# Kernel optimization log

Hardware: AMD Instinct MI355X
Metric: run time of the kernel (lower is better)

## Reference

```python
import jax, jax.numpy as jnp
import numpy as np

B, L, D, H, SD = 8, 1024, 768, 12, 5
DK = D // H
PAD = 256  # last PAD keys are padding


def _lin(key, fan_in, fan_out):
    kw, kb = jax.random.split(key)
    s = 1.0 / np.sqrt(fan_in)
    w = jax.random.uniform(kw, (fan_in, fan_out), jnp.float32, -s, s)
    b = jax.random.uniform(kb, (fan_out,), jnp.float32, -s, s)
    return w, b


def setup_inputs() -> dict:
    key = jax.random.key(0)
    ks = jax.random.split(key, 10)
    w_q, b_q = _lin(ks[0], D, D)
    w_k, b_k = _lin(ks[1], D, D)
    w_v, b_v = _lin(ks[2], D, D)
    w_fc, b_fc = _lin(ks[3], D, D)
    w_loc, b_loc = _lin(ks[4], SD, H)
    return {
        'q': jax.random.normal(ks[5], (B, L, D), jnp.float32),
        'k': jax.random.normal(ks[6], (B, L, D), jnp.float32),
        'v': jax.random.normal(ks[7], (B, L, D), jnp.float32),
        'pairwise_locs': jax.random.normal(ks[8], (B, L, L, SD), jnp.float32),
        'key_padding_mask': jnp.broadcast_to(jnp.arange(L) >= (L - PAD), (B, L)),
        'w_q': w_q, 'b_q': b_q, 'w_k': w_k, 'b_k': b_k,
        'w_v': w_v, 'b_v': b_v, 'w_fc': w_fc, 'b_fc': b_fc,
        'w_loc': w_loc, 'b_loc': b_loc,
        'ln_g': jnp.ones((D,), jnp.float32), 'ln_b': jnp.zeros((D,), jnp.float32),
    }


def _split_heads(x):  # [b, t, D] -> [h, b, t, dk]
    b, t, _ = x.shape
    return x.reshape(b, t, H, DK).transpose(2, 0, 1, 3)


def reference(q, k, v, pairwise_locs, key_padding_mask,
              w_q, b_q, w_k, b_k, w_v, b_v, w_fc, b_fc,
              w_loc, b_loc, ln_g, ln_b):
    residual = q
    qh = _split_heads(q @ w_q + b_q)   # h b l k
    kh = _split_heads(k @ w_k + b_k)   # h b t k
    vh = _split_heads(v @ w_v + b_v)   # h b t v
    scale = 1.0 / jnp.sqrt(jnp.asarray(DK, qh.dtype))
    attn = jnp.einsum('hblk,hbtk->hblt', qh, kh) * scale
    # pairwise_loc_fc: [b,l,t,sd] @ [sd,h] + b -> rearrange to h b l t; 'mul' fusion uses relu
    loc_attn = jax.nn.relu(jnp.einsum('bltd,dh->hblt', pairwise_locs, w_loc)
                           + b_loc[:, None, None, None])
    m = key_padding_mask[None, :, None, :]  # h b l t broadcast
    attn = jnp.where(m, -jnp.inf, attn)
    loc_attn = jnp.where(m, 0.0, loc_attn)
    fused_attn = jax.nn.softmax(jnp.log(jnp.clip(loc_attn, 1e-6)) + attn, axis=3)
    out = jnp.einsum('hblt,hbtv->hblv', fused_attn, vh)
    out = out.transpose(1, 2, 0, 3).reshape(q.shape[0], q.shape[1], D)
    out = out @ w_fc + b_fc  # dropout is identity in eval
    x = out + residual
    mu = jnp.mean(x, -1, keepdims=True)
    var = jnp.var(x, -1, keepdims=True)
    out = (x - mu) / jnp.sqrt(var + 1e-5) * ln_g + ln_b
    return (out, fused_attn)
```

## Files before the change

kernel.cpp:

```cpp
#include <hip/hip_runtime.h>
#include <hip/hip_bf16.h>

constexpr int B_  = 8;
constexpr int L_  = 1024;
constexpr int D_  = 768;
constexpr int H_  = 12;
constexpr int DK_ = 64;
constexpr int SD_ = 5;
constexpr int VALID_ = 768;

constexpr float SSCALE_ = 0.18033688011112042f;

typedef __attribute__((ext_vector_type(8))) __bf16 bf16x8;
typedef __attribute__((ext_vector_type(4))) float floatx4;

__device__ __forceinline__ unsigned short f2bf(float f) {
    unsigned int u = __float_as_uint(f);
    unsigned int r = (u + 0x7FFFu + ((u >> 16) & 1u)) >> 16;
    return (unsigned short)r;
}

__device__ __forceinline__ void g2l16(const void* g, void* l) {
    __builtin_amdgcn_global_load_lds(
        (const __attribute__((address_space(1))) void*)g,
        (__attribute__((address_space(3))) void*)l, 16, 0, 0);
}

__global__ __launch_bounds__(256) void cvt3_kernel(
    const float* __restrict__ x0, const float* __restrict__ x1,
    const float* __restrict__ x2,
    unsigned short* __restrict__ o0, unsigned short* __restrict__ o1,
    unsigned short* __restrict__ o2)
{
    const int w = blockIdx.y;
    const float* x = (w == 0) ? x0 : (w == 1) ? x1 : x2;
    unsigned short* o = (w == 0) ? o0 : (w == 1) ? o1 : o2;
    size_t i = ((size_t)blockIdx.x * 256 + threadIdx.x) * 8;
    float4 a = *(const float4*)(x + i);
    float4 b = *(const float4*)(x + i + 4);
    ushort4 q1; q1.x = f2bf(a.x); q1.y = f2bf(a.y); q1.z = f2bf(a.z); q1.w = f2bf(a.w);
    ushort4 q2; q2.x = f2bf(b.x); q2.y = f2bf(b.y); q2.z = f2bf(b.z); q2.w = f2bf(b.w);
    *(ushort4*)(o + i) = q1;
    *(ushort4*)(o + i + 4) = q2;
}

__global__ __launch_bounds__(256) void wt4_kernel(
    const float* __restrict__ W0, const float* __restrict__ W1,
    const float* __restrict__ W2, const float* __restrict__ W3,
    unsigned short* __restrict__ T0, unsigned short* __restrict__ T1,
    unsigned short* __restrict__ T2, unsigned short* __restrict__ T3)
{
    const int w = blockIdx.z;
    const float* W = (w == 0) ? W0 : (w == 1) ? W1 : (w == 2) ? W2 : W3;
    unsigned short* Wt = (w == 0) ? T0 : (w == 1) ? T1 : (w == 2) ? T2 : T3;
    __shared__ float tl[64][65];
    const int k0 = blockIdx.x * 64, n0 = blockIdx.y * 64;
    const int tid = threadIdx.x;
    #pragma unroll
    for (int i = 0; i < 4; i++) {
        int c = tid + i * 256;
        int r = c >> 4, c4 = (c & 15) * 4;
        float4 v = *(const float4*)(W + (size_t)(k0 + r) * D_ + n0 + c4);
        tl[r][c4] = v.x; tl[r][c4 + 1] = v.y; tl[r][c4 + 2] = v.z; tl[r][c4 + 3] = v.w;
    }
    __syncthreads();
    #pragma unroll
    for (int i = 0; i < 4; i++) {
        int c = tid + i * 256;
        int n_ = c >> 4, k4 = (c & 15) * 4;
        ushort4 o;
        o.x = f2bf(tl[k4 + 0][n_]); o.y = f2bf(tl[k4 + 1][n_]);
        o.z = f2bf(tl[k4 + 2][n_]); o.w = f2bf(tl[k4 + 3][n_]);
        *(ushort4*)(Wt + (size_t)(n0 + n_) * D_ + k0 + k4) = o;
    }
}

__global__ __launch_bounds__(256) void vt_kernel(
    const unsigned short* __restrict__ Vh, unsigned short* __restrict__ Vt)
{
    __shared__ unsigned short tl[64][65];
    const int t0 = blockIdx.x * 64, hb = blockIdx.y;
    const int tid = threadIdx.x;
    const unsigned short* src = Vh + (size_t)hb * L_ * DK_ + (size_t)t0 * DK_;
    #pragma unroll
    for (int i = 0; i < 4; i++) {
        int c = tid + i * 256;
        int r = c >> 4, c4 = (c & 15) * 4;
        ushort4 v = *(const ushort4*)(src + r * DK_ + c4);
        tl[r][c4] = v.x; tl[r][c4 + 1] = v.y; tl[r][c4 + 2] = v.z; tl[r][c4 + 3] = v.w;
    }
    __syncthreads();
    unsigned short* dst = Vt + (size_t)hb * DK_ * VALID_ + t0;
    #pragma unroll
    for (int i = 0; i < 4; i++) {
        int c = tid + i * 256;
        int dk = c >> 4, t4 = (c & 15) * 4;
        ushort4 o;
        o.x = tl[t4 + 0][dk]; o.y = tl[t4 + 1][dk];
        o.z = tl[t4 + 2][dk]; o.w = tl[t4 + 3][dk];
        *(ushort4*)(dst + (size_t)dk * VALID_ + t4) = o;
    }
}

__global__ __launch_bounds__(256) void gemm_proj3(
    const unsigned short* __restrict__ A0, const unsigned short* __restrict__ A1,
    const unsigned short* __restrict__ A2,
    const unsigned short* __restrict__ B0, const unsigned short* __restrict__ B1,
    const unsigned short* __restrict__ B2,
    const float* __restrict__ bias0, const float* __restrict__ bias1,
    const float* __restrict__ bias2,
    unsigned short* __restrict__ O0, unsigned short* __restrict__ O1,
    unsigned short* __restrict__ O2)
{
    const int which = blockIdx.z;
    const unsigned short* Abf = (which == 0) ? A0 : (which == 1) ? A1 : A2;
    const unsigned short* Bt  = (which == 0) ? B0 : (which == 1) ? B1 : B2;
    const float* bias         = (which == 0) ? bias0 : (which == 1) ? bias1 : bias2;
    unsigned short* out       = (which == 0) ? O0 : (which == 1) ? O1 : O2;

    __shared__ __align__(16) __bf16 As[128 * 32];
    __shared__ __align__(16) __bf16 Bs[128 * 32];
    const int tid = threadIdx.x;
    const int f = blockIdx.x + 6 * blockIdx.y;
    const int xcd = f & 7, j5 = f >> 3;
    const int n0 = (j5 % 6) * 128;
    const int m0 = (xcd * 8 + j5 / 6) * 128;
    const int lane = tid & 63, wv = tid >> 6;
    const int quad = lane >> 4, ln15 = lane & 15;
    const int wm = (wv >> 1) * 64, wn = (wv & 1) * 64;
    const __bf16* Ap = (const __bf16*)Abf + (size_t)m0 * D_;
    const __bf16* Bp = (const __bf16*)Bt + (size_t)n0 * D_;
    floatx4 acc[4][4];
    #pragma unroll
    for (int i = 0; i < 4; i++)
        #pragma unroll
        for (int j = 0; j < 4; j++) acc[i][j] = (floatx4)0.f;

    for (int k0 = 0; k0 < D_; k0 += 32) {
        #pragma unroll
        for (int j = 0; j < 2; j++) {
            int c = tid + j * 256;
            g2l16(Ap + (size_t)(c >> 2) * D_ + k0 + (c & 3) * 8, As + c * 8);
            g2l16(Bp + (size_t)(c >> 2) * D_ + k0 + (c & 3) * 8, Bs + c * 8);
        }
        __syncthreads();
        bf16x8 af[4], bfr[4];
        #pragma unroll
        for (int i = 0; i < 4; i++)
            af[i] = *(const bf16x8*)(As + (wm + i * 16 + ln15) * 32 + quad * 8);
        #pragma unroll
        for (int i = 0; i < 4; i++)
            bfr[i] = *(const bf16x8*)(Bs + (wn + i * 16 + ln15) * 32 + quad * 8);
        #pragma unroll
        for (int i = 0; i < 4; i++)
            #pragma unroll
            for (int j = 0; j < 4; j++)
                acc[i][j] = __builtin_amdgcn_mfma_f32_16x16x32_bf16(af[i], bfr[j], acc[i][j], 0, 0, 0);
        __syncthreads();
    }
    #pragma unroll
    for (int ni = 0; ni < 4; ni++) {
        int n = n0 + wn + ni * 16 + ln15;
        int h = n >> 6, dk = n & 63;
        float bv = bias[n];
        #pragma unroll
        for (int mi = 0; mi < 4; mi++)
            #pragma unroll
            for (int r = 0; r < 4; r++) {
                int m = m0 + wm + mi * 16 + quad * 4 + r;
                int b = m >> 10, l = m & 1023;
                out[(((size_t)h * B_ + b) * L_ + l) * DK_ + dk] = f2bf(acc[mi][ni][r] + bv);
            }
    }
}

__global__ __launch_bounds__(256) void gemm_fc(
    const unsigned short* __restrict__ Abf, const unsigned short* __restrict__ Bt,
    const float* __restrict__ bias, const float* __restrict__ resid,
    float* __restrict__ out)
{
    __shared__ __align__(16) __bf16 As[128 * 32];
    __shared__ __align__(16) __bf16 Bs[128 * 32];
    const int tid = threadIdx.x;
    const int f = blockIdx.x + 6 * blockIdx.y;
    const int xcd = f & 7, j5 = f >> 3;
    const int n0 = (j5 % 6) * 128;
    const int m0 = (xcd * 8 + j5 / 6) * 128;
    const int lane = tid & 63, wv = tid >> 6;
    const int quad = lane >> 4, ln15 = lane & 15;
    const int wm = (wv >> 1) * 64, wn = (wv & 1) * 64;
    const __bf16* Ap = (const __bf16*)Abf + (size_t)m0 * D_;
    const __bf16* Bp = (const __bf16*)Bt + (size_t)n0 * D_;
    floatx4 acc[4][4];
    #pragma unroll
    for (int i = 0; i < 4; i++)
        #pragma unroll
        for (int j = 0; j < 4; j++) acc[i][j] = (floatx4)0.f;

    for (int k0 = 0; k0 < D_; k0 += 32) {
        #pragma unroll
        for (int j = 0; j < 2; j++) {
            int c = tid + j * 256;
            g2l16(Ap + (size_t)(c >> 2) * D_ + k0 + (c & 3) * 8, As + c * 8);
            g2l16(Bp + (size_t)(c >> 2) * D_ + k0 + (c & 3) * 8, Bs + c * 8);
        }
        __syncthreads();
        bf16x8 af[4], bfr[4];
        #pragma unroll
        for (int i = 0; i < 4; i++)
            af[i] = *(const bf16x8*)(As + (wm + i * 16 + ln15) * 32 + quad * 8);
        #pragma unroll
        for (int i = 0; i < 4; i++)
            bfr[i] = *(const bf16x8*)(Bs + (wn + i * 16 + ln15) * 32 + quad * 8);
        #pragma unroll
        for (int i = 0; i < 4; i++)
            #pragma unroll
            for (int j = 0; j < 4; j++)
                acc[i][j] = __builtin_amdgcn_mfma_f32_16x16x32_bf16(af[i], bfr[j], acc[i][j], 0, 0, 0);
        __syncthreads();
    }
    #pragma unroll
    for (int ni = 0; ni < 4; ni++) {
        int n = n0 + wn + ni * 16 + ln15;
        float bv = bias[n];
        #pragma unroll
        for (int mi = 0; mi < 4; mi++)
            #pragma unroll
            for (int r = 0; r < 4; r++) {
                int m = m0 + wm + mi * 16 + quad * 4 + r;
                size_t off = (size_t)m * D_ + n;
                out[off] = acc[mi][ni][r] + bv + resid[off];
            }
    }
}

__global__ __launch_bounds__(768) void fused_s_kernel(
    const unsigned short* __restrict__ Qh, const unsigned short* __restrict__ Kh,
    const float* __restrict__ ploc, const float* __restrict__ w_loc,
    const float* __restrict__ b_loc,
    unsigned short* __restrict__ U, float* __restrict__ invZ)
{
    const int id = blockIdx.x;
    const int b = id & 7, l0 = (id >> 3) * 32;
    const int tid = threadIdx.x;
    const int h = tid >> 6, lane = tid & 63;
    const int quad = lane >> 4, ln15 = lane & 15;
    __shared__ __align__(16) float pl[32 * 320];

    const float w0 = w_loc[0 * H_ + h], w1 = w_loc[1 * H_ + h],
                w2 = w_loc[2 * H_ + h], w3 = w_loc[3 * H_ + h],
                w4 = w_loc[4 * H_ + h], bh = b_loc[h];

    const __bf16* Qp = (const __bf16*)Qh + (((size_t)h * B_ + b) * L_ + l0) * DK_;
    const __bf16* Kp = (const __bf16*)Kh + (((size_t)h * B_ + b) * L_) * DK_;
    unsigned short* Ub = U + (((size_t)h * B_ + b) * L_ + l0) * VALID_;
    const float* plsrc = ploc + ((size_t)(b * L_ + l0) * L_) * SD_;

    bf16x8 af[2][2];
    #pragma unroll
    for (int mi = 0; mi < 2; mi++)
        #pragma unroll
        for (int kk = 0; kk < 2; kk++)
            af[mi][kk] = *(const bf16x8*)(Qp + (size_t)(mi * 16 + ln15) * DK_ + kk * 32 + quad * 8);

    float zp[2][4];
    #pragma unroll
    for (int mi = 0; mi < 2; mi++)
        #pragma unroll
        for (int r = 0; r < 4; r++) zp[mi][r] = 0.f;

    for (int t0 = 0; t0 < VALID_; t0 += 64) {
        __syncthreads();
        #pragma unroll
        for (int i = 0; i < 4; i++) {
            int jj = tid + i * 768;
            if (jj < 2560) {
                int l = jj / 80, off = (jj % 80) * 4;
                g2l16(plsrc + (size_t)l * L_ * SD_ + t0 * SD_ + off, pl + l * 320 + off);
            }
        }
        __syncthreads();

        floatx4 acc[2][4];
        #pragma unroll
        for (int mi = 0; mi < 2; mi++)
            #pragma unroll
            for (int ni = 0; ni < 4; ni++) acc[mi][ni] = (floatx4)0.f;
        bf16x8 bfr[4][2];
        #pragma unroll
        for (int ni = 0; ni < 4; ni++)
            #pragma unroll
            for (int kk = 0; kk < 2; kk++)
                bfr[ni][kk] = *(const bf16x8*)(Kp + (size_t)(t0 + ni * 16 + ln15) * DK_ + kk * 32 + quad * 8);
        #pragma unroll
        for (int kk = 0; kk < 2; kk++)
            #pragma unroll
            for (int mi = 0; mi < 2; mi++)
                #pragma unroll
                for (int ni = 0; ni < 4; ni++)
                    acc[mi][ni] = __builtin_amdgcn_mfma_f32_16x16x32_bf16(af[mi][kk], bfr[ni][kk], acc[mi][ni], 0, 0, 0);

        #pragma unroll
        for (int ni = 0; ni < 4; ni++) {
            int t = ni * 16 + ln15;
            #pragma unroll
            for (int mi = 0; mi < 2; mi++)
                #pragma unroll
                for (int r = 0; r < 4; r++) {
                    int lrow = mi * 16 + quad * 4 + r;
                    const float* pp = pl + lrow * 320 + t * 5;
                    float c = bh + pp[0] * w0 + pp[1] * w1 + pp[2] * w2
                                 + pp[3] * w3 + pp[4] * w4;
                    c = fmaxf(c, 1e-6f);
                    float u = c * exp2f(acc[mi][ni][r] * SSCALE_);
                    zp[mi][r] += u;
                    Ub[(size_t)lrow * VALID_ + t0 + t] = f2bf(u);
                }
        }
    }
    #pragma unroll
    for (int m = 1; m < 16; m <<= 1)
        #pragma unroll
        for (int mi = 0; mi < 2; mi++)
            #pragma unroll
            for (int r = 0; r < 4; r++)
                zp[mi][r] += __shfl_xor(zp[mi][r], m, 64);
    if (ln15 == 0) {
        #pragma unroll
        for (int mi = 0; mi < 2; mi++)
            #pragma unroll
            for (int r = 0; r < 4; r++) {
                int lrow = mi * 16 + quad * 4 + r;
                invZ[((size_t)h * B_ + b) * L_ + l0 + lrow] = 1.f / zp[mi][r];
            }
    }
}

__global__ __launch_bounds__(256) void gemm_pv(
    const unsigned short* __restrict__ P, const unsigned short* __restrict__ Vt,
    const float* __restrict__ invZ,
    unsigned short* __restrict__ attn, float* __restrict__ fused)
{
    __shared__ __align__(16) __bf16 As[128 * 32];
    __shared__ __align__(16) __bf16 Bs[64 * 32];
    __shared__ float zrow[128];
    const int tid = threadIdx.x;
    const int f = blockIdx.x + 8 * blockIdx.y;
    const int xcd = f & 7, j5 = f >> 3;
    const int hb = xcd * 12 + (j5 % 12);
    const int m0 = (j5 / 12) * 128;
    const int h = hb >> 3, b = hb & 7;
    const int lane = tid & 63, wv = tid >> 6;
    const int quad = lane >> 4, ln15 = lane & 15;
    const int wm = (wv >> 1) * 64, wn = (wv & 1) * 32;
    const __bf16* Ap = (const __bf16*)P + (size_t)hb * L_ * VALID_ + (size_t)m0 * VALID_;
    const __bf16* Bp = (const __bf16*)Vt + (size_t)hb * DK_ * VALID_;
    float* fbase = fused + ((size_t)hb * L_ + m0) * L_;
    if (tid < 128) zrow[tid] = invZ[(size_t)hb * L_ + m0 + tid];
    floatx4 acc[4][2];
    #pragma unroll
    for (int i = 0; i < 4; i++)
        #pragma unroll
        for (int j = 0; j < 2; j++) acc[i][j] = (floatx4)0.f;

    for (int k0 = 0; k0 < VALID_; k0 += 32) {
        #pragma unroll
        for (int j = 0; j < 2; j++) {
            int c = tid + j * 256;
            g2l16(Ap + (size_t)(c >> 2) * VALID_ + k0 + (c & 3) * 8, As + c * 8);
        }
        {
            int c = tid;
            g2l16(Bp + (size_t)(c >> 2) * VALID_ + k0 + (c & 3) * 8, Bs + c * 8);
        }
        __syncthreads();
        {
            int row = tid >> 1, half = tid & 1;
            const __bf16* src = As + row * 32 + half * 16;
            float iz = zrow[row];
            bf16x8 v0 = *(const bf16x8*)(src);
            bf16x8 v1 = *(const bf16x8*)(src + 8);
            float* dst = fbase + (size_t)row * L_ + k0 + half * 16;
            #pragma unroll
            for (int jj = 0; jj < 8; jj++) dst[jj] = (float)v0[jj] * iz;
            #pragma unroll
            for (int jj = 0; jj < 8; jj++) dst[8 + jj] = (float)v1[jj] * iz;
        }
        bf16x8 af[4], bfr[2];
        #pragma unroll
        for (int i = 0; i < 4; i++)
            af[i] = *(const bf16x8*)(As + (wm + i * 16 + ln15) * 32 + quad * 8);
        #pragma unroll
        for (int i = 0; i < 2; i++)
            bfr[i] = *(const bf16x8*)(Bs + (wn + i * 16 + ln15) * 32 + quad * 8);
        #pragma unroll
        for (int i = 0; i < 4; i++)
            #pragma unroll
            for (int j = 0; j < 2; j++)
                acc[i][j] = __builtin_amdgcn_mfma_f32_16x16x32_bf16(af[i], bfr[j], acc[i][j], 0, 0, 0);
        __syncthreads();
    }
    {
        float4 z4 = make_float4(0.f, 0.f, 0.f, 0.f);
        #pragma unroll
        for (int i = 0; i < 32; i++) {
            int idx = tid + i * 256;
            int row = idx >> 6, c = (idx & 63) * 4;
            *(float4*)(fbase + (size_t)row * L_ + VALID_ + c) = z4;
        }
    }
    #pragma unroll
    for (int ni = 0; ni < 2; ni++) {
        int dk = wn + ni * 16 + ln15;
        #pragma unroll
        for (int mi = 0; mi < 4; mi++)
            #pragma unroll
            for (int r = 0; r < 4; r++) {
                int mloc = wm + mi * 16 + quad * 4 + r;
                int m = m0 + mloc;
                attn[((size_t)b * L_ + m) * D_ + h * DK_ + dk] =
                    f2bf(acc[mi][ni][r] * zrow[mloc]);
            }
    }
}

__global__ __launch_bounds__(256) void ln_kernel(
    float* __restrict__ x, const float* __restrict__ g, const float* __restrict__ bb)
{
    const int r = blockIdx.x, tid = threadIdx.x;
    float* row = x + (size_t)r * D_;
    float v0 = row[tid], v1 = row[tid + 256], v2 = row[tid + 512];
    float s = v0 + v1 + v2;
    float s2 = v0 * v0 + v1 * v1 + v2 * v2;
    #pragma unroll
    for (int off = 32; off > 0; off >>= 1) {
        s  += __shfl_down(s, off, 64);
        s2 += __shfl_down(s2, off, 64);
    }
    __shared__ float rs[4], rs2[4], mb[2];
    const int lane = tid & 63, wid = tid >> 6;
    if (lane == 0) { rs[wid] = s; rs2[wid] = s2; }
    __syncthreads();
    if (tid == 0) {
        float S = rs[0] + rs[1] + rs[2] + rs[3];
        float S2 = rs2[0] + rs2[1] + rs2[2] + rs2[3];
        float mean = S * (1.f / 768.f);
        float var = S2 * (1.f / 768.f) - mean * mean;
        mb[0] = mean; mb[1] = rsqrtf(var + 1e-5f);
    }
    __syncthreads();
    float mean = mb[0], rstd = mb[1];
    row[tid]       = (v0 - mean) * rstd * g[tid]       + bb[tid];
    row[tid + 256] = (v1 - mean) * rstd * g[tid + 256] + bb[tid + 256];
    row[tid + 512] = (v2 - mean) * rstd * g[tid + 512] + bb[tid + 512];
}

extern "C" void kernel_launch(void* const* d_in, const int* in_sizes, int n_in,
                              void* d_out, int out_size, void* d_ws, size_t ws_size,
                              hipStream_t stream)
{
    const float* q     = (const float*)d_in[0];
    const float* k     = (const float*)d_in[1];
    const float* v     = (const float*)d_in[2];
    const float* ploc  = (const float*)d_in[3];
    const float* w_q   = (const float*)d_in[5];
    const float* b_q   = (const float*)d_in[6];
    const float* w_k   = (const float*)d_in[7];
    const float* b_k   = (const float*)d_in[8];
    const float* w_v   = (const float*)d_in[9];
    const float* b_v   = (const float*)d_in[10];
    const float* w_fc  = (const float*)d_in[11];
    const float* b_fc  = (const float*)d_in[12];
    const float* w_loc = (const float*)d_in[13];
    const float* b_loc = (const float*)d_in[14];
    const float* ln_g  = (const float*)d_in[15];
    const float* ln_b  = (const float*)d_in[16];

    float* out   = (float*)d_out;
    float* fused = out + (size_t)B_ * L_ * D_;

    constexpr size_t NHE = (size_t)H_ * B_ * L_ * DK_;
    constexpr size_t NVT = (size_t)H_ * B_ * DK_ * VALID_;
    constexpr size_t NW  = (size_t)D_ * D_;
    constexpr size_t NP  = (size_t)H_ * B_ * L_ * VALID_;
    unsigned short* Qh   = (unsigned short*)d_ws;
    unsigned short* Kh   = Qh + NHE;
    unsigned short* Vh   = Kh + NHE;
    unsigned short* Vt   = Vh + NHE;
    unsigned short* Xq   = Vt + NVT;
    unsigned short* Xk   = Xq + NHE;
    unsigned short* Xv   = Xk + NHE;
    unsigned short* WqT  = Xv + NHE;
    unsigned short* WkT  = WqT + NW;
    unsigned short* WvT  = WkT + NW;
    unsigned short* WfcT = WvT + NW;
    unsigned short* Pb   = WfcT + NW;
    unsigned short* AObf = Pb + NP;
    float* Zb            = (float*)(AObf + NHE);

    cvt3_kernel<<<dim3(3072, 3), 256, 0, stream>>>(q, k, v, Xq, Xk, Xv);
    wt4_kernel<<<dim3(12, 12, 4), 256, 0, stream>>>(w_q, w_k, w_v, w_fc, WqT, WkT, WvT, WfcT);
    gemm_proj3<<<dim3(6, 64, 3), 256, 0, stream>>>(
        Xq, Xk, Xv, WqT, WkT, WvT, b_q, b_k, b_v, Qh, Kh, Vh);
    vt_kernel<<<dim3(12, 96), 256, 0, stream>>>(Vh, Vt);
    fused_s_kernel<<<256, 768, 0, stream>>>(Qh, Kh, ploc, w_loc, b_loc, Pb, Zb);
    gemm_pv<<<dim3(8, 96), 256, 0, stream>>>(Pb, Vt, Zb, AObf, fused);
    gemm_fc<<<dim3(6, 64), 256, 0, stream>>>(AObf, WfcT, b_fc, q, out);
    ln_kernel<<<dim3(B_ * L_), 256, 0, stream>>>(out, ln_g, ln_b);
}
```

Before: 904.8 us.

## Precompute per-head location bias once per tile in LDS and prefetch locs into registers

Instead of each head's wave recomputing the 5-term location projection from fp32 locs staged in LDS, threads compute all 12 heads' clamped projections once per (l,t) and store them as bf16 in a shared table. The next tile's locs are software-prefetched into registers while the MFMA work runs. K fragments are loaded per kk to reduce register pressure, and occupancy is hinted with launch_bounds(768,3). The bf16 rounding of the location term adds a small precision loss, and the prefetch reads locs past column 768 on the final iteration. Those extra reads stay inside the tensor but are wasted work.

```diff
diff --git a/kernel.cpp b/kernel.cpp
--- a/kernel.cpp
+++ b/kernel.cpp
@@ -18,6 +18,10 @@
     unsigned int u = __float_as_uint(f);
     unsigned int r = (u + 0x7FFFu + ((u >> 16) & 1u)) >> 16;
     return (unsigned short)r;
+}
+
+__device__ __forceinline__ float bf2f(unsigned short us) {
+    return __uint_as_float((unsigned int)us << 16);
 }
 
 __device__ __forceinline__ void g2l16(const void* g, void* l) {
@@ -234,7 +238,7 @@
     }
 }
 
-__global__ __launch_bounds__(768) void fused_s_kernel(
+__global__ __launch_bounds__(768, 3) void fused_s_kernel(
     const unsigned short* __restrict__ Qh, const unsigned short* __restrict__ Kh,
     const float* __restrict__ ploc, const float* __restrict__ w_loc,
     const float* __restrict__ b_loc,
@@ -245,11 +249,16 @@
     const int tid = threadIdx.x;
     const int h = tid >> 6, lane = tid & 63;
     const int quad = lane >> 4, ln15 = lane & 15;
-    __shared__ __align__(16) float pl[32 * 320];
-
-    const float w0 = w_loc[0 * H_ + h], w1 = w_loc[1 * H_ + h],
-                w2 = w_loc[2 * H_ + h], w3 = w_loc[3 * H_ + h],
-                w4 = w_loc[4 * H_ + h], bh = b_loc[h];
+    constexpr int CS = 64 * 12 + 8;
+    __shared__ unsigned short ct[32 * CS];
+
+    float wl[SD_][H_], blh[H_];
+    #pragma unroll
+    for (int d = 0; d < SD_; d++)
+        #pragma unroll
+        for (int hh = 0; hh < H_; hh++) wl[d][hh] = w_loc[d * H_ + hh];
+    #pragma unroll
+    for (int hh = 0; hh < H_; hh++) blh[hh] = b_loc[hh];
 
     const __bf16* Qp = (const __bf16*)Qh + (((size_t)h * B_ + b) * L_ + l0) * DK_;
     const __bf16* Kp = (const __bf16*)Kh + (((size_t)h * B_ + b) * L_) * DK_;
@@ -263,6 +272,18 @@
         for (int kk = 0; kk < 2; kk++)
             af[mi][kk] = *(const bf16x8*)(Qp + (size_t)(mi * 16 + ln15) * DK_ + kk * 32 + quad * 8);
 
+    float pv5[3][5];
+    #pragma unroll
+    for (int p = 0; p < 3; p++) {
+        int jj = tid + p * 768;
+        if (jj < 2048) {
+            int l = jj >> 6, tt = jj & 63;
+            const float* lp = plsrc + (size_t)l * L_ * SD_ + tt * SD_;
+            #pragma unroll
+            for (int d = 0; d < 5; d++) pv5[p][d] = lp[d];
+        }
+    }
+
     float zp[2][4];
     #pragma unroll
     for (int mi = 0; mi < 2; mi++)
@@ -272,34 +293,48 @@
     for (int t0 = 0; t0 < VALID_; t0 += 64) {
         __syncthreads();
         #pragma unroll
-        for (int i = 0; i < 4; i++) {
-            int jj = tid + i * 768;
-            if (jj < 2560) {
-                int l = jj / 80, off = (jj % 80) * 4;
-                g2l16(plsrc + (size_t)l * L_ * SD_ + t0 * SD_ + off, pl + l * 320 + off);
+        for (int p = 0; p < 3; p++) {
+            int jj = tid + p * 768;
+            if (jj < 2048) {
+                int l = jj >> 6, tt = jj & 63;
+                #pragma unroll
+                for (int hh = 0; hh < H_; hh++) {
+                    float c = blh[hh] + pv5[p][0] * wl[0][hh] + pv5[p][1] * wl[1][hh]
+                            + pv5[p][2] * wl[2][hh] + pv5[p][3] * wl[3][hh]
+                            + pv5[p][4] * wl[4][hh];
+                    ct[l * CS + tt * 12 + hh] = f2bf(fmaxf(c, 1e-6f));
+                }
             }
         }
         __syncthreads();
 
+        #pragma unroll
+        for (int p = 0; p < 3; p++) {
+            int jj = tid + p * 768;
+            if (jj < 2048) {
+                int l = jj >> 6, tt = jj & 63;
+                const float* lp = plsrc + (size_t)l * L_ * SD_ + (t0 + 64 + tt) * SD_;
+                #pragma unroll
+                for (int d = 0; d < 5; d++) pv5[p][d] = lp[d];
+            }
+        }
         floatx4 acc[2][4];
         #pragma unroll
         for (int mi = 0; mi < 2; mi++)
             #pragma unroll
             for (int ni = 0; ni < 4; ni++) acc[mi][ni] = (floatx4)0.f;
-        bf16x8 bfr[4][2];
-        #pragma unroll
-        for (int ni = 0; ni < 4; ni++)
-            #pragma unroll
-            for (int kk = 0; kk < 2; kk++)
-                bfr[ni][kk] = *(const bf16x8*)(Kp + (size_t)(t0 + ni * 16 + ln15) * DK_ + kk * 32 + quad * 8);
-        #pragma unroll
-        for (int kk = 0; kk < 2; kk++)
+        #pragma unroll
+        for (int kk = 0; kk < 2; kk++) {
+            bf16x8 bfr[4];
+            #pragma unroll
+            for (int ni = 0; ni < 4; ni++)
+                bfr[ni] = *(const bf16x8*)(Kp + (size_t)(t0 + ni * 16 + ln15) * DK_ + kk * 32 + quad * 8);
             #pragma unroll
             for (int mi = 0; mi < 2; mi++)
                 #pragma unroll
                 for (int ni = 0; ni < 4; ni++)
-                    acc[mi][ni] = __builtin_amdgcn_mfma_f32_16x16x32_bf16(af[mi][kk], bfr[ni][kk], acc[mi][ni], 0, 0, 0);
-
+                    acc[mi][ni] = __builtin_amdgcn_mfma_f32_16x16x32_bf16(af[mi][kk], bfr[ni], acc[mi][ni], 0, 0, 0);
+        }
         #pragma unroll
         for (int ni = 0; ni < 4; ni++) {
             int t = ni * 16 + ln15;
@@ -308,10 +343,7 @@
                 #pragma unroll
                 for (int r = 0; r < 4; r++) {
                     int lrow = mi * 16 + quad * 4 + r;
-                    const float* pp = pl + lrow * 320 + t * 5;
-                    float c = bh + pp[0] * w0 + pp[1] * w1 + pp[2] * w2
-                                 + pp[3] * w3 + pp[4] * w4;
-                    c = fmaxf(c, 1e-6f);
+                    float c = bf2f(ct[lrow * CS + t * 12 + h]);
                     float u = c * exp2f(acc[mi][ni][r] * SSCALE_);
                     zp[mi][r] += u;
                     Ub[(size_t)lrow * VALID_ + t0 + t] = f2bf(u);
```

Result: faster. 882.6 us (-2.4%).
